# Optimization experiments

Measured on AMD Instinct MI355X. Metric: run time of the kernel, lower is better.

## Reference

```python
import jax, jax.numpy as jnp
import numpy as np

B, C_IN, N, T, E, C_OUT = 128, 32, 325, 24, 3, 64


def setup_inputs() -> dict:
    key = jax.random.key(0)
    kx, ka, kw, kb = jax.random.split(key, 4)
    x = jax.random.normal(kx, (B, C_IN, N, T), dtype=jnp.float32)
    supports = jax.random.normal(ka, (E, N, N), dtype=jnp.float32) * (1.0 / np.sqrt(N))
    # 1x1 Conv2d params: weight [c_out, c_in*(edge_dim+1)], bias [c_out]
    fan_in = C_IN * (E + 1)
    W = jax.random.normal(kw, (C_OUT, fan_in), dtype=jnp.float32) * (1.0 / np.sqrt(fan_in))
    b = jax.random.normal(kb, (C_OUT,), dtype=jnp.float32) * 0.05
    return {"x": x, "supports": supports, "W": W, "b": b}


def reference(x, supports, W, b):
    # x: [B, C, N, T], supports: [E, N, N]
    Bb, C, Nn, Tt = x.shape
    # nconv for every support at once: einsum 'bcvt,vw->bcwt' batched over E
    diff = jnp.einsum('bcvt,evw->becwt', x, supports)  # [B, E, C, N, T]
    # concat [x] + diffused copies along channel dim -> [B, (E+1)*C, N, T]
    h = jnp.concatenate([x[:, None], diff], axis=1).reshape(Bb, -1, Nn, Tt)
    # 1x1 conv == channel-mixing matmul; squeeze(-1) is a no-op since T > 1
    out = jnp.einsum('bkvt,ok->bovt', h, W) + b[None, :, None, None]
    return out  # [B, c_out, N, T]
```

## Files before the change

### kernel.cpp

```cpp
#include <hip/hip_runtime.h>
#include <hip/hip_bf16.h>

typedef short bf16x8 __attribute__((ext_vector_type(8)));
typedef short bf16x4 __attribute__((ext_vector_type(4)));
typedef float f32x4  __attribute__((ext_vector_type(4)));

static constexpr int Bb   = 128;
static constexpr int Cin  = 32;
static constexpr int Nn   = 325;
static constexpr int Tt   = 24;
static constexpr int Cout = 64;
static constexpr int NKS  = 11;
static constexpr int WP   = 336;
static constexpr int NWT  = 21;
static constexpr size_t XTB_ELEMS = (size_t)Bb * NKS * (Tt * Cin) * 32;
static constexpr size_t STP_ELEMS = (size_t)3 * NKS * WP * 32;
static constexpr size_t WB_ELEMS  = (size_t)Cout * 128;

__device__ __forceinline__ void gld16(const void* g, void* l) {
    __builtin_amdgcn_global_load_lds(
        (const __attribute__((address_space(1))) void*)g,
        (__attribute__((address_space(3))) void*)l, 16, 0, 0);
}
__device__ __forceinline__ short bfb(float f) {
    __hip_bfloat16 h = __float2bfloat16(f);
    return *reinterpret_cast<short*>(&h);
}

__global__ void build_tabs(const float* __restrict__ sup,
                           const float* __restrict__ W,
                           __hip_bfloat16* __restrict__ stpb,
                           __hip_bfloat16* __restrict__ Wb) {
    int idx = blockIdx.x * 256 + threadIdx.x;
    int total = 3 * NKS * WP * 32;
    if (idx < total) {
        int ep = idx / (NKS * WP * 32);
        int r  = idx % (NKS * WP * 32);
        int ks = r / (WP * 32);
        int r2 = r % (WP * 32);
        int w  = r2 / 32;
        int vi = r2 % 32;
        int v  = ks * 32 + vi;
        float val = 0.f;
        if (v < Nn && w < Nn)
            val = sup[((size_t)ep * Nn + v) * Nn + w];
        stpb[idx] = __float2bfloat16(val);
    } else {
        int wi = idx - total;
        if (wi < Cout * 128) Wb[wi] = __float2bfloat16(W[wi]);
    }
}

__global__ void transpose_x(const float* __restrict__ x,
                            __hip_bfloat16* __restrict__ xTb) {
    __shared__ __hip_bfloat16 ls[Cin * 32 * 28];
    int xcd = blockIdx.x & 7;
    int idx = blockIdx.x >> 3;
    int b   = xcd * 16 + idx / NKS;
    int ks  = idx % NKS;
    int tid = threadIdx.x;
    for (int i = 0; i < 24; ++i) {
        int f4 = i * 256 + tid;
        int c  = f4 / 192;
        int rm = f4 % 192;
        int vi = rm / 6;
        int t0 = (rm % 6) * 4;
        int v  = ks * 32 + vi;
        float4 val = make_float4(0.f, 0.f, 0.f, 0.f);
        if (v < Nn)
            val = *(const float4*)(x + (((size_t)(b * Cin + c) * Nn + v) * Tt + t0));
        bf16x4 pk = { bfb(val.x), bfb(val.y), bfb(val.z), bfb(val.w) };
        *(bf16x4*)&ls[(c * 32 + vi) * 28 + t0] = pk;
    }
    __syncthreads();
    for (int j = 0; j < 12; ++j) {
        int o    = j * 256 + tid;
        int row  = o >> 2;
        int slot = o & 3;
        int t = row >> 5, c = row & 31;
        union { short us[8]; bf16x8 v8; } pk;
#pragma unroll
        for (int q = 0; q < 8; ++q) {
            __hip_bfloat16 h = ls[(c * 32 + slot * 8 + q) * 28 + t];
            pk.us[q] = *reinterpret_cast<short*>(&h);
        }
        *(bf16x8*)((char*)xTb + ((size_t)(b * NKS + ks) * 768 + row) * 64 + slot * 16) = pk.v8;
    }
}

__global__ __launch_bounds__(384, 3) void graphconv_main(
    const __hip_bfloat16* __restrict__ xTb,
    const __hip_bfloat16* __restrict__ stpb,
    const __hip_bfloat16* __restrict__ Wb,
    const float* __restrict__ bias,
    float* __restrict__ out) {
    __shared__ alignas(16) char smem[49152 + 32768];
    char*  ring = smem;
    char*  Ss   = smem + 49152;
    float* Os   = (float*)smem;

    int bid = blockIdx.x;
    int lg  = (bid & 7) * 672 + (bid >> 3);
    int b   = lg / 42;
    int r   = lg % 42;
    int wt  = r >> 1, th = r & 1;
    int w0  = wt * 16;

    int tid = threadIdx.x, wid = tid >> 6, lane = tid & 63;
    int cl = lane & 15, kg = lane >> 4;

    int srow  = lane >> 2;
    int sslot = ((lane & 3) ^ ((lane >> 3) & 3)) << 4;
    const int asw = (kg ^ ((cl >> 1) & 3)) << 4;

    const char* xslab = (const char*)xTb + (size_t)b * NKS * 768 * 64;
    const char* xsrc  = xslab + (size_t)(th * 384 + wid * 64 + srow) * 64 + sslot;
    char*       xdst  = ring + wid * 4096 + lane * 16;

    for (int i = wid; i < 32; i += 6) {
        gld16((const char*)stpb + ((size_t)i * WP + w0 + srow) * 64 + sslot,
              Ss + i * 1024 + lane * 16);
    }
    bf16x8 afk10 = *(const bf16x8*)((const char*)stpb +
                       ((size_t)32 * WP + w0 + cl) * 64 + kg * 16);
#pragma unroll
    for (int s = 0; s < 2; ++s)
#pragma unroll
        for (int q = 0; q < 4; ++q)
            gld16(xsrc + (size_t)s * 49152 + q * 1024,
                  xdst + s * 24576 + q * 1024);

    bf16x8 idf;
    {
        short hot = (kg == 2 * (wt & 1) + (cl >> 3)) ? (short)0x3F80 : (short)0;
        bf16x8 z = { 0, 0, 0, 0, 0, 0, 0, 0 };
#pragma unroll
        for (int i = 0; i < 8; ++i)
            z[i] = (i == (cl & 7)) ? hot : (short)0;
        idf = z;
    }
    const int id_ks = wt >> 1;

    asm volatile("s_waitcnt vmcnt(9)" ::: "memory");
    __builtin_amdgcn_sched_barrier(0);
    __builtin_amdgcn_s_barrier();

    f32x4 acc1[3][4] = {};
    f32x4 aid[4]     = {};
#pragma unroll
    for (int ks = 0; ks < NKS; ++ks) {
        if (ks < 10) { asm volatile("s_waitcnt vmcnt(4)" ::: "memory"); }
        else         { asm volatile("s_waitcnt vmcnt(0)" ::: "memory"); }
        __builtin_amdgcn_sched_barrier(0);
        const int bsel = (ks & 1) * 24576;
        bf16x8 xf[4];
#pragma unroll
        for (int j = 0; j < 4; ++j)
            xf[j] = *(const bf16x8*)(ring + bsel + wid * 4096 + j * 1024 +
                                     cl * 64 + asw);
        asm volatile("s_waitcnt lgkmcnt(0)" ::: "memory");
        __builtin_amdgcn_sched_barrier(0);
        if (ks < 9) {
#pragma unroll
            for (int q = 0; q < 4; ++q)
                gld16(xsrc + (size_t)(ks + 2) * 49152 + q * 1024,
                      xdst + bsel + q * 1024);
        }
        bf16x8 af[3];
#pragma unroll
        for (int ep = 0; ep < 3; ++ep) {
            int slab = ep * NKS + ks;
            af[ep] = (slab < 32)
                ? *(const bf16x8*)(Ss + slab * 1024 + cl * 64 + asw)
                : afk10;
        }
#pragma unroll
        for (int ep = 0; ep < 3; ++ep)
#pragma unroll
            for (int j = 0; j < 4; ++j)
                acc1[ep][j] = __builtin_amdgcn_mfma_f32_16x16x32_bf16(
                    xf[j], af[ep], acc1[ep][j], 0, 0, 0);
        if (ks == id_ks) {
#pragma unroll
            for (int j = 0; j < 4; ++j)
                aid[j] = __builtin_amdgcn_mfma_f32_16x16x32_bf16(
                    xf[j], idf, aid[j], 0, 0, 0);
        }
    }

    f32x4 acc2[4][2] = {};
#pragma unroll
    for (int kappa = 0; kappa < 8; ++kappa) {
        const int es = kappa >> 1, half = kappa & 1;
        bf16x4 wf[4];
#pragma unroll
        for (int mt = 0; mt < 4; ++mt)
            wf[mt] = *(const bf16x4*)((const char*)Wb + (mt * 16 + cl) * 256 +
                                      kappa * 32 + kg * 8);
#pragma unroll
        for (int tj = 0; tj < 2; ++tj) {
            const int j = tj * 2 + half;
            f32x4 y = (es == 0) ? aid[j] : acc1[es - 1][j];
            bf16x4 pb = { bfb(y[0]), bfb(y[1]), bfb(y[2]), bfb(y[3]) };
#pragma unroll
            for (int mt = 0; mt < 4; ++mt)
                acc2[mt][tj] = __builtin_amdgcn_mfma_f32_16x16x16bf16_1k(
                    wf[mt], pb, acc2[mt][tj], 0, 0, 0);
        }
    }

    __builtin_amdgcn_s_barrier();
#pragma unroll
    for (int p = 0; p < 2; ++p) {
        if (p) {
            asm volatile("s_waitcnt lgkmcnt(0)" ::: "memory");
            __builtin_amdgcn_s_barrier();
        }
#pragma unroll
        for (int mh = 0; mh < 2; ++mh) {
            const int mt = p * 2 + mh;
#pragma unroll
            for (int tj = 0; tj < 2; ++tj) {
                const int t = wid * 2 + tj;
#pragma unroll
                for (int r2_ = 0; r2_ < 4; ++r2_)
                    Os[(mh * 16 + kg * 4 + r2_) * 208 + cl * 13 + t] =
                        acc2[mt][tj][r2_];
            }
        }
        asm volatile("s_waitcnt lgkmcnt(0)" ::: "memory");
        __builtin_amdgcn_s_barrier();
        for (int pair = tid; pair < 512; pair += 384) {
            const int o2 = pair >> 4, w = pair & 15;
            const int wg = w0 + w;
            if (wg < Nn) {
                const int o = p * 32 + o2;
                const float bv = bias[o];
                float f[12];
#pragma unroll
                for (int q = 0; q < 12; ++q)
                    f[q] = Os[o2 * 208 + w * 13 + q] + bv;
                float* op = out + ((size_t)(b * Cout + o) * Nn + wg) * Tt + th * 12;
#pragma unroll
                for (int q3 = 0; q3 < 3; ++q3)
                    *(float4*)(op + q3 * 4) = make_float4(
                        f[q3 * 4], f[q3 * 4 + 1], f[q3 * 4 + 2], f[q3 * 4 + 3]);
            }
        }
    }
}

extern "C" void kernel_launch(void* const* d_in, const int* in_sizes, int n_in,
                              void* d_out, int out_size, void* d_ws, size_t ws_size,
                              hipStream_t stream) {
    const float* x    = (const float*)d_in[0];
    const float* sup  = (const float*)d_in[1];
    const float* W    = (const float*)d_in[2];
    const float* bias = (const float*)d_in[3];
    float* out = (float*)d_out;

    __hip_bfloat16* xTb  = (__hip_bfloat16*)d_ws;
    __hip_bfloat16* stpb = xTb + XTB_ELEMS;
    __hip_bfloat16* Wb   = stpb + STP_ELEMS;

    int build_total = (int)(STP_ELEMS + WB_ELEMS);
    build_tabs<<<(build_total + 255) / 256, 256, 0, stream>>>(sup, W, stpb, Wb);
    transpose_x<<<Bb * NKS, 256, 0, stream>>>(x, xTb);
    graphconv_main<<<Bb * NWT * 2, 384, 0, stream>>>(xTb, stpb, Wb, bias, out);
}
```

Measured before the change: 328.6 us.

## Replace identity MFMA with direct x gather and shrink LDS support staging

Result: slower. 338.1 us (+2.9%).

```diff
diff --git a/kernel.cpp b/kernel.cpp
--- a/kernel.cpp
+++ b/kernel.cpp
@@ -94,7 +94,7 @@
     const __hip_bfloat16* __restrict__ Wb,
     const float* __restrict__ bias,
     float* __restrict__ out) {
-    __shared__ alignas(16) char smem[49152 + 32768];
+    __shared__ alignas(16) char smem[49152 + 29696];
     char*  ring = smem;
     char*  Ss   = smem + 49152;
     float* Os   = (float*)smem;
@@ -117,12 +117,22 @@
     const char* xsrc  = xslab + (size_t)(th * 384 + wid * 64 + srow) * 64 + sslot;
     char*       xdst  = ring + wid * 4096 + lane * 16;
 
-    for (int i = wid; i < 32; i += 6) {
+    for (int i = wid; i < 29; i += 6) {
         gld16((const char*)stpb + ((size_t)i * WP + w0 + srow) * 64 + sslot,
               Ss + i * 1024 + lane * 16);
     }
-    bf16x8 afk10 = *(const bf16x8*)((const char*)stpb +
-                       ((size_t)32 * WP + w0 + cl) * 64 + kg * 16);
+    bf16x8 afk[4];
+#pragma unroll
+    for (int i = 0; i < 4; ++i)
+        afk[i] = *(const bf16x8*)((const char*)stpb +
+                     ((size_t)(29 + i) * WP + w0 + cl) * 64 + kg * 16);
+#pragma unroll
+    for (int i = 0; i < 4; ++i)
+        asm volatile("" : "+v"(afk[i]));
+    asm volatile("s_waitcnt vmcnt(0)" ::: "memory");
+    __builtin_amdgcn_sched_barrier(0);
+    __builtin_amdgcn_s_barrier();
+
 #pragma unroll
     for (int s = 0; s < 2; ++s)
 #pragma unroll
@@ -130,23 +140,7 @@
             gld16(xsrc + (size_t)s * 49152 + q * 1024,
                   xdst + s * 24576 + q * 1024);
 
-    bf16x8 idf;
-    {
-        short hot = (kg == 2 * (wt & 1) + (cl >> 3)) ? (short)0x3F80 : (short)0;
-        bf16x8 z = { 0, 0, 0, 0, 0, 0, 0, 0 };
-#pragma unroll
-        for (int i = 0; i < 8; ++i)
-            z[i] = (i == (cl & 7)) ? hot : (short)0;
-        idf = z;
-    }
-    const int id_ks = wt >> 1;
-
-    asm volatile("s_waitcnt vmcnt(9)" ::: "memory");
-    __builtin_amdgcn_sched_barrier(0);
-    __builtin_amdgcn_s_barrier();
-
     f32x4 acc1[3][4] = {};
-    f32x4 aid[4]     = {};
 #pragma unroll
     for (int ks = 0; ks < NKS; ++ks) {
         if (ks < 10) { asm volatile("s_waitcnt vmcnt(4)" ::: "memory"); }
@@ -169,10 +163,10 @@
         bf16x8 af[3];
 #pragma unroll
         for (int ep = 0; ep < 3; ++ep) {
-            int slab = ep * NKS + ks;
-            af[ep] = (slab < 32)
+            const int slab = ep * NKS + ks;
+            af[ep] = (slab < 29)
                 ? *(const bf16x8*)(Ss + slab * 1024 + cl * 64 + asw)
-                : afk10;
+                : afk[slab - 29];
         }
 #pragma unroll
         for (int ep = 0; ep < 3; ++ep)
@@ -180,12 +174,18 @@
             for (int j = 0; j < 4; ++j)
                 acc1[ep][j] = __builtin_amdgcn_mfma_f32_16x16x32_bf16(
                     xf[j], af[ep], acc1[ep][j], 0, 0, 0);
-        if (ks == id_ks) {
-#pragma unroll
-            for (int j = 0; j < 4; ++j)
-                aid[j] = __builtin_amdgcn_mfma_f32_16x16x32_bf16(
-                    xf[j], idf, aid[j], 0, 0, 0);
-        }
+    }
+
+    const char* xid = xslab + (size_t)(wt >> 1) * 49152 +
+                      (size_t)(16 * (wt & 1) + cl) * 2;
+    bf16x4 pbx[4];
+#pragma unroll
+    for (int j = 0; j < 4; ++j) {
+        const char* rp = xid + (size_t)((th * 12 + wid * 2 + (j >> 1)) * 32 +
+                                        (j & 1) * 16 + kg * 4) * 64;
+        bf16x4 p = { *(const short*)(rp),       *(const short*)(rp + 64),
+                     *(const short*)(rp + 128), *(const short*)(rp + 192) };
+        pbx[j] = p;
     }
 
     f32x4 acc2[4][2] = {};
@@ -200,8 +200,14 @@
 #pragma unroll
         for (int tj = 0; tj < 2; ++tj) {
             const int j = tj * 2 + half;
-            f32x4 y = (es == 0) ? aid[j] : acc1[es - 1][j];
-            bf16x4 pb = { bfb(y[0]), bfb(y[1]), bfb(y[2]), bfb(y[3]) };
+            bf16x4 pb;
+            if (es == 0) {
+                pb = pbx[j];
+            } else {
+                f32x4 y = acc1[es - 1][j];
+                bf16x4 t4 = { bfb(y[0]), bfb(y[1]), bfb(y[2]), bfb(y[3]) };
+                pb = t4;
+            }
 #pragma unroll
             for (int mt = 0; mt < 4; ++mt)
                 acc2[mt][tj] = __builtin_amdgcn_mfma_f32_16x16x16bf16_1k(
```
